# Kernel optimization log

Measured on AMD Instinct MI355X. Metric: run time of the kernel, lower is better.

Reference implementation:

```python
import jax, jax.numpy as jnp
import numpy as np

M, N, D = 8192, 8192, 64

def setup_inputs() -> dict:
    key = jax.random.key(0)
    k1, k2 = jax.random.split(key)
    X = jax.random.normal(k1, (M, D), dtype=jnp.float32)
    Y = jax.random.normal(k2, (N, D), dtype=jnp.float32)
    gamma_param = jnp.asarray(1.0, dtype=jnp.float32)  # learnable scalar (rbf branch)
    return {"X": X, "Y": Y, "gamma_param": gamma_param}

def reference(X, Y, gamma_param):
    # RBF kernel: exp(-gamma * ||x_i - y_j||^2), (m, n)
    x_sq = jnp.sum(X * X, axis=-1)          # (m,)
    y_sq = jnp.sum(Y * Y, axis=-1)          # (n,)
    xy = jnp.einsum("md,nd->mn", X, Y)      # (m, n)
    sq_norm = x_sq[:, None] + y_sq[None, :] - 2.0 * xy
    sq_norm = jnp.maximum(sq_norm, 0.0)     # numerical clamp
    return jnp.exp(-gamma_param * sq_norm)
```

## Files before the change

### kernel.cpp

```cpp
#include <hip/hip_runtime.h>

#define MTOT 8192
#define NTOT 8192
#define DD   64
#define SPLIT (MTOT * DD)

typedef __bf16 bf16x8 __attribute__((ext_vector_type(8)));
typedef float  f32x16 __attribute__((ext_vector_type(16)));
typedef unsigned short u16;
typedef unsigned short u16x4 __attribute__((ext_vector_type(4)));
typedef unsigned short u16x8 __attribute__((ext_vector_type(8)));

__device__ __forceinline__ u16 bf16_rne(float v) {
    unsigned int u = __float_as_uint(v);
    u = u + 0x7FFFu + ((u >> 16) & 1u);
    return (u16)(u >> 16);
}
__device__ __forceinline__ float bf16_to_f32(u16 h) {
    return __uint_as_float(((unsigned int)h) << 16);
}

#define MFMA(a, b, c) __builtin_amdgcn_mfma_f32_32x32x16_bf16((a), (b), (c), 0, 0, 0)

__global__ __launch_bounds__(256)
void rbf_pre_kernel(const float* __restrict__ X, const float* __restrict__ Y,
                    u16* __restrict__ XhiF, u16* __restrict__ XloF,
                    u16* __restrict__ YhiF, u16* __restrict__ YloF,
                    float* __restrict__ xqs, float* __restrict__ yqs)
{
    const int gid = blockIdx.x * 256 + threadIdx.x;
    const int mat = gid >> 15;
    const int r4  = gid & 32767;
    const int row = r4 >> 2;
    const int q   = r4 & 3;
    const float* src = mat ? Y : X;
    u16* hi  = mat ? YhiF : XhiF;
    u16* lo  = mat ? YloF : XloF;
    float* nrm = mat ? yqs : xqs;

    const long rbase = (long)row * DD + q * 16;
    float s = 0.f;
    u16x8 h0, h1, l0, l1;
    #pragma unroll
    for (int c = 0; c < 4; ++c) {
        const float4 v = *reinterpret_cast<const float4*>(src + rbase + c * 4);
        const float vv[4] = {v.x, v.y, v.z, v.w};
        #pragma unroll
        for (int e = 0; e < 4; ++e) {
            const int idx = c * 4 + e;
            const float x = vv[e];
            s = fmaf(x, x, s);
            const u16 hh = bf16_rne(x);
            const u16 ll = bf16_rne(x - bf16_to_f32(hh));
            if (idx < 8) { h0[idx] = hh; l0[idx] = ll; }
            else         { h1[idx - 8] = hh; l1[idx - 8] = ll; }
        }
    }
    s += __shfl_xor(s, 1);
    s += __shfl_xor(s, 2);
    if (q == 0) nrm[row] = s;

    const int tt = row >> 5, lr = row & 31;
    const long fbase = (long)(tt * 4 + q) * 512;
    *reinterpret_cast<u16x8*>(hi + fbase + lr * 8)        = h0;
    *reinterpret_cast<u16x8*>(hi + fbase + (32 + lr) * 8) = h1;
    *reinterpret_cast<u16x8*>(lo + fbase + lr * 8)        = l0;
    *reinterpret_cast<u16x8*>(lo + fbase + (32 + lr) * 8) = l1;
}

__global__ __launch_bounds__(256, 2)
void rbf_rowslab_kernel(const u16* __restrict__ XhiF, const u16* __restrict__ XloF,
                        const u16* __restrict__ YhiF, const u16* __restrict__ YloF,
                        const float* __restrict__ xqs, const float* __restrict__ yqs,
                        const float* __restrict__ gamma_p,
                        float* __restrict__ out)
{
    __shared__ __align__(16) u16 S[4][8192];

    const int t = threadIdx.x;
    const int w = t >> 6;
    const int l = t & 63;
    const int loff = l * 8;

    const int bid = blockIdx.x;
    const int swz = ((bid & 7) << 9) | (bid >> 3);
    const int bm = swz >> 6;
    const int bn = swz & 63;
    const long row0 = (long)bm * 128;
    const long col0 = (long)bn * 128;

    {
        const u16* gsrc;
        if      (w == 0) gsrc = XhiF + (long)bm * 8192;
        else if (w == 1) gsrc = XloF + (long)bm * 8192;
        else if (w == 2) gsrc = YhiF + (long)bn * 8192;
        else             gsrc = YloF + (long)bn * 8192;
        u16* const ldst = &S[w][0];
        #pragma unroll
        for (int c = 0; c < 16; ++c) {
            const int off = c * 512 + loff;
            *reinterpret_cast<int4*>(ldst + off) = *reinterpret_cast<const int4*>(gsrc + off);
        }
    }

    const float g  = gamma_p[0];
    const float g2 = 2.0f * g;
    const int l5x4 = (l >> 5) * 4;
    const int  ln  = l & 31;

    float xv[16];
    #pragma unroll
    for (int q4 = 0; q4 < 4; ++q4) {
        const float4 x4 = *reinterpret_cast<const float4*>(
            xqs + row0 + w * 32 + 8 * q4 + l5x4);
        xv[q4 * 4 + 0] = x4.x; xv[q4 * 4 + 1] = x4.y;
        xv[q4 * 4 + 2] = x4.z; xv[q4 * 4 + 3] = x4.w;
    }
    const float cy0 = -g * yqs[col0 +  0 + ln];
    const float cy1 = -g * yqs[col0 + 32 + ln];
    const float cy2 = -g * yqs[col0 + 64 + ln];
    const float cy3 = -g * yqs[col0 + 96 + ln];

    __syncthreads();

    bf16x8 aH[4], aL[4];
    #pragma unroll
    for (int ks = 0; ks < 4; ++ks) {
        aH[ks] = *reinterpret_cast<const bf16x8*>(&S[0][(w * 4 + ks) * 512 + loff]);
        aL[ks] = *reinterpret_cast<const bf16x8*>(&S[1][(w * 4 + ks) * 512 + loff]);
    }

    f32x16 q0, q1, q2, q3;
    #pragma unroll
    for (int r = 0; r < 16; ++r) { q0[r] = 0.f; q1[r] = 0.f; q2[r] = 0.f; q3[r] = 0.f; }

#define QUAD(ACC, JJ)                                                                   \
    {                                                                                   \
        bf16x8 bh[4], bl[4];                                                            \
        _Pragma("unroll")                                                               \
        for (int ks = 0; ks < 4; ++ks) {                                                \
            bh[ks] = *reinterpret_cast<const bf16x8*>(&S[2][((JJ) * 4 + ks) * 512 + loff]); \
            bl[ks] = *reinterpret_cast<const bf16x8*>(&S[3][((JJ) * 4 + ks) * 512 + loff]); \
        }                                                                               \
        _Pragma("unroll")                                                               \
        for (int ks = 0; ks < 4; ++ks) {                                                \
            ACC = MFMA(aH[ks], bh[ks], ACC);                                            \
            ACC = MFMA(aH[ks], bl[ks], ACC);                                            \
            ACC = MFMA(aL[ks], bh[ks], ACC);                                            \
        }                                                                               \
    }

    QUAD(q0, 0)
    QUAD(q1, 1)
    QUAD(q2, 2)
    QUAD(q3, 3)
#undef QUAD

    float* const obase = out + (row0 + w * 32) * (long)NTOT + col0 + ln;
    #pragma unroll
    for (int r = 0; r < 16; ++r) {
        const int rr = (r & 3) + 8 * (r >> 2) + l5x4;
        float* const orow = obase + rr * (long)NTOT;
        const float nx = -g * xv[r];
        const float a0 = fminf(fmaf(g2, q0[r], nx + cy0), 0.f);
        const float a1 = fminf(fmaf(g2, q1[r], nx + cy1), 0.f);
        const float a2 = fminf(fmaf(g2, q2[r], nx + cy2), 0.f);
        const float a3 = fminf(fmaf(g2, q3[r], nx + cy3), 0.f);
        __builtin_nontemporal_store(__expf(a0), orow);
        __builtin_nontemporal_store(__expf(a1), orow + 32);
        __builtin_nontemporal_store(__expf(a2), orow + 64);
        __builtin_nontemporal_store(__expf(a3), orow + 96);
    }
}

__global__ __launch_bounds__(256, 2)
void rbf_fallback_kernel(const float* __restrict__ X,
                         const float* __restrict__ Y,
                         const float* __restrict__ gamma_p,
                         float* __restrict__ out)
{
    __shared__ unsigned short XfH[4][4][64][8];
    __shared__ unsigned short XfL[4][4][64][8];
    __shared__ unsigned short YfH[4][4][64][8];
    __shared__ unsigned short YfL[4][4][64][8];
    __shared__ float xq[128];
    __shared__ float yq[128];

    const int t = threadIdx.x;
    const long row0 = (long)blockIdx.y * 128;
    const long col0 = (long)blockIdx.x * 128;

    {
        const int k0   = (t & 15) * 4;
        const int ks   = k0 >> 4;
        const int l32  = ((k0 >> 3) & 1) << 5;
        const int slot = k0 & 4;
        #pragma unroll
        for (int i = 0; i < 8; ++i) {
            const int row  = (t >> 4) + i * 16;
            const int mt   = row >> 5;
            const int lane = (row & 31) | l32;
            const float4 vx = *reinterpret_cast<const float4*>(X + (row0 + row) * DD + k0);
            const float4 vy = *reinterpret_cast<const float4*>(Y + (col0 + row) * DD + k0);
            float xv[4] = {vx.x, vx.y, vx.z, vx.w};
            float yv[4] = {vy.x, vy.y, vy.z, vy.w};
            u16x4 xh, xl, yh, yl;
            #pragma unroll
            for (int e = 0; e < 4; ++e) {
                const u16 hx = bf16_rne(xv[e]);
                xh[e] = hx; xl[e] = bf16_rne(xv[e] - bf16_to_f32(hx));
                const u16 hy = bf16_rne(yv[e]);
                yh[e] = hy; yl[e] = bf16_rne(yv[e] - bf16_to_f32(hy));
            }
            *reinterpret_cast<u16x4*>(&XfH[mt][ks][lane][slot]) = xh;
            *reinterpret_cast<u16x4*>(&XfL[mt][ks][lane][slot]) = xl;
            *reinterpret_cast<u16x4*>(&YfH[mt][ks][lane][slot]) = yh;
            *reinterpret_cast<u16x4*>(&YfL[mt][ks][lane][slot]) = yl;
        }
    }
    {
        const int r = t & 127;
        const float* p2 = (t < 128) ? (X + (row0 + r) * DD) : (Y + (col0 + r) * DD);
        float s0 = 0.f, s1 = 0.f, s2 = 0.f, s3 = 0.f;
        #pragma unroll
        for (int c = 0; c < 16; ++c) {
            const float4 v = reinterpret_cast<const float4*>(p2)[c];
            s0 = fmaf(v.x, v.x, s0); s1 = fmaf(v.y, v.y, s1);
            s2 = fmaf(v.z, v.z, s2); s3 = fmaf(v.w, v.w, s3);
        }
        const float s = (s0 + s1) + (s2 + s3);
        if (t < 128) xq[r] = s; else yq[r] = s;
    }
    __syncthreads();

    const int w = t >> 6;
    const int l = t & 63;
    const int mt0 = (w >> 1) * 2;
    const int nt0 = (w & 1) * 2;

    bf16x8 aH[2][4], aL[2][4];
    #pragma unroll
    for (int i = 0; i < 2; ++i)
        #pragma unroll
        for (int ks = 0; ks < 4; ++ks) {
            aH[i][ks] = *reinterpret_cast<const bf16x8*>(&XfH[mt0 + i][ks][l][0]);
            aL[i][ks] = *reinterpret_cast<const bf16x8*>(&XfL[mt0 + i][ks][l][0]);
        }

    f32x16 acc[2][2];
    #pragma unroll
    for (int i = 0; i < 2; ++i)
        #pragma unroll
        for (int j = 0; j < 2; ++j)
            #pragma unroll
            for (int r = 0; r < 16; ++r) acc[i][j][r] = 0.f;

    #pragma unroll
    for (int ks = 0; ks < 4; ++ks) {
        const bf16x8 b0h = *reinterpret_cast<const bf16x8*>(&YfH[nt0 + 0][ks][l][0]);
        const bf16x8 b1h = *reinterpret_cast<const bf16x8*>(&YfH[nt0 + 1][ks][l][0]);
        const bf16x8 b0l = *reinterpret_cast<const bf16x8*>(&YfL[nt0 + 0][ks][l][0]);
        const bf16x8 b1l = *reinterpret_cast<const bf16x8*>(&YfL[nt0 + 1][ks][l][0]);
        acc[0][0] = MFMA(aH[0][ks], b0h, acc[0][0]);
        acc[0][1] = MFMA(aH[0][ks], b1h, acc[0][1]);
        acc[1][0] = MFMA(aH[1][ks], b0h, acc[1][0]);
        acc[1][1] = MFMA(aH[1][ks], b1h, acc[1][1]);
        acc[0][0] = MFMA(aH[0][ks], b0l, acc[0][0]);
        acc[0][1] = MFMA(aH[0][ks], b1l, acc[0][1]);
        acc[1][0] = MFMA(aH[1][ks], b0l, acc[1][0]);
        acc[1][1] = MFMA(aH[1][ks], b1l, acc[1][1]);
        acc[0][0] = MFMA(aL[0][ks], b0h, acc[0][0]);
        acc[0][1] = MFMA(aL[0][ks], b1h, acc[0][1]);
        acc[1][0] = MFMA(aL[1][ks], b0h, acc[1][0]);
        acc[1][1] = MFMA(aL[1][ks], b1h, acc[1][1]);
    }

    const float g = gamma_p[0];
    const int l5x4 = (l >> 5) * 4;
    const int ln = l & 31;
    #pragma unroll
    for (int i = 0; i < 2; ++i) {
        const int mt = mt0 + i;
        float xv[16];
        #pragma unroll
        for (int r = 0; r < 16; ++r)
            xv[r] = xq[mt * 32 + (r & 3) + 8 * (r >> 2) + l5x4];
        #pragma unroll
        for (int j = 0; j < 2; ++j) {
            const int nt = nt0 + j;
            const float yv = yq[nt * 32 + ln];
            const long gr = row0 + mt * 32;
            const long gc = col0 + nt * 32 + ln;
            #pragma unroll
            for (int r = 0; r < 16; ++r) {
                float s = fmaf(-2.f, acc[i][j][r], xv[r] + yv);
                s = fmaxf(s, 0.f);
                const long rr = gr + (r & 3) + 8 * (r >> 2) + l5x4;
                out[rr * NTOT + gc] = __expf(-g * s);
            }
        }
    }
}

extern "C" void kernel_launch(void* const* d_in, const int* in_sizes, int n_in,
                              void* d_out, int out_size, void* d_ws, size_t ws_size,
                              hipStream_t stream) {
    (void)in_sizes; (void)n_in; (void)out_size;
    const float* X = (const float*)d_in[0];
    const float* Y = (const float*)d_in[1];
    const float* gamma_p = (const float*)d_in[2];
    float* out = (float*)d_out;

    const size_t need = 4 * (size_t)SPLIT * sizeof(u16) + (MTOT + NTOT) * sizeof(float);

    if (ws_size >= need) {
        u16* XhiF = (u16*)d_ws;
        u16* XloF = XhiF + SPLIT;
        u16* YhiF = XloF + SPLIT;
        u16* YloF = YhiF + SPLIT;
        float* xqs = (float*)(YloF + SPLIT);
        float* yqs = xqs + MTOT;
        rbf_pre_kernel<<<256, 256, 0, stream>>>(X, Y, XhiF, XloF, YhiF, YloF, xqs, yqs);
        rbf_rowslab_kernel<<<4096, 256, 0, stream>>>(XhiF, XloF, YhiF, YloF, xqs, yqs, gamma_p, out);
    } else {
        dim3 grid(NTOT / 128, MTOT / 128);
        rbf_fallback_kernel<<<grid, 256, 0, stream>>>(X, Y, gamma_p, out);
    }
}
```

Before: 61.74 us.

## Shrink block tile to 64x128 with direct-global A fragments for higher occupancy

Replaces the 128x128 row-slab kernel with a 64x128 tile kernel that stages only the Y hi/lo fragments in shared memory. Each wave loads its X hi/lo fragments directly from global memory and computes a 32x64 sub-tile with two accumulators instead of four. Shared memory per block is halved and the launch bound is raised to 4 blocks per CU, and the grid doubles to 8192 blocks. The aim is more concurrent waves to hide the latency of the output stores, in exchange for more total reads of Y across blocks and less data reuse per block.

```diff
diff --git a/kernel.cpp b/kernel.cpp
--- a/kernel.cpp
+++ b/kernel.cpp
@@ -68,14 +68,14 @@
     *reinterpret_cast<u16x8*>(lo + fbase + (32 + lr) * 8) = l1;
 }
 
-__global__ __launch_bounds__(256, 2)
-void rbf_rowslab_kernel(const u16* __restrict__ XhiF, const u16* __restrict__ XloF,
-                        const u16* __restrict__ YhiF, const u16* __restrict__ YloF,
-                        const float* __restrict__ xqs, const float* __restrict__ yqs,
-                        const float* __restrict__ gamma_p,
-                        float* __restrict__ out)
+__global__ __launch_bounds__(256, 4)
+void rbf_hiocc_kernel(const u16* __restrict__ XhiF, const u16* __restrict__ XloF,
+                      const u16* __restrict__ YhiF, const u16* __restrict__ YloF,
+                      const float* __restrict__ xqs, const float* __restrict__ yqs,
+                      const float* __restrict__ gamma_p,
+                      float* __restrict__ out)
 {
-    __shared__ __align__(16) u16 S[4][8192];
+    __shared__ __align__(16) u16 S[2][8192];
 
     const int t = threadIdx.x;
     const int w = t >> 6;
@@ -83,24 +83,33 @@
     const int loff = l * 8;
 
     const int bid = blockIdx.x;
-    const int swz = ((bid & 7) << 9) | (bid >> 3);
+    const int swz = ((bid & 7) << 10) | (bid >> 3);
     const int bm = swz >> 6;
     const int bn = swz & 63;
-    const long row0 = (long)bm * 128;
+    const long row0 = (long)bm * 64;
     const long col0 = (long)bn * 128;
 
     {
-        const u16* gsrc;
-        if      (w == 0) gsrc = XhiF + (long)bm * 8192;
-        else if (w == 1) gsrc = XloF + (long)bm * 8192;
-        else if (w == 2) gsrc = YhiF + (long)bn * 8192;
-        else             gsrc = YloF + (long)bn * 8192;
-        u16* const ldst = &S[w][0];
-        #pragma unroll
-        for (int c = 0; c < 16; ++c) {
-            const int off = c * 512 + loff;
-            *reinterpret_cast<int4*>(ldst + off) = *reinterpret_cast<const int4*>(gsrc + off);
-        }
+        const u16* const yh = YhiF + (long)bn * 8192;
+        const u16* const yl = YloF + (long)bn * 8192;
+        #pragma unroll
+        for (int cc = 0; cc < 8; ++cc) {
+            const int c = w * 8 + cc;
+            const u16* gsrc = (c < 16) ? (yh + c * 512) : (yl + (c - 16) * 512);
+            u16* ldst = (c < 16) ? &S[0][c * 512] : &S[1][(c - 16) * 512];
+            *reinterpret_cast<int4*>(ldst + loff) = *reinterpret_cast<const int4*>(gsrc + loff);
+        }
+    }
+
+    const int mt  = w & 1;
+    const int nt0 = (w >> 1) * 2;
+
+    const long att = (long)(bm * 2 + mt);
+    bf16x8 aH[4], aL[4];
+    #pragma unroll
+    for (int ks = 0; ks < 4; ++ks) {
+        aH[ks] = *reinterpret_cast<const bf16x8*>(XhiF + (att * 4 + ks) * 512 + loff);
+        aL[ks] = *reinterpret_cast<const bf16x8*>(XloF + (att * 4 + ks) * 512 + loff);
     }
 
     const float g  = gamma_p[0];
@@ -112,64 +121,42 @@
     #pragma unroll
     for (int q4 = 0; q4 < 4; ++q4) {
         const float4 x4 = *reinterpret_cast<const float4*>(
-            xqs + row0 + w * 32 + 8 * q4 + l5x4);
+            xqs + row0 + mt * 32 + 8 * q4 + l5x4);
         xv[q4 * 4 + 0] = x4.x; xv[q4 * 4 + 1] = x4.y;
         xv[q4 * 4 + 2] = x4.z; xv[q4 * 4 + 3] = x4.w;
     }
-    const float cy0 = -g * yqs[col0 +  0 + ln];
-    const float cy1 = -g * yqs[col0 + 32 + ln];
-    const float cy2 = -g * yqs[col0 + 64 + ln];
-    const float cy3 = -g * yqs[col0 + 96 + ln];
+    const float cy0 = -g * yqs[col0 + (nt0 + 0) * 32 + ln];
+    const float cy1 = -g * yqs[col0 + (nt0 + 1) * 32 + ln];
 
     __syncthreads();
 
-    bf16x8 aH[4], aL[4];
+    f32x16 acc0, acc1;
+    #pragma unroll
+    for (int r = 0; r < 16; ++r) { acc0[r] = 0.f; acc1[r] = 0.f; }
+
     #pragma unroll
     for (int ks = 0; ks < 4; ++ks) {
-        aH[ks] = *reinterpret_cast<const bf16x8*>(&S[0][(w * 4 + ks) * 512 + loff]);
-        aL[ks] = *reinterpret_cast<const bf16x8*>(&S[1][(w * 4 + ks) * 512 + loff]);
-    }
-
-    f32x16 q0, q1, q2, q3;
-    #pragma unroll
-    for (int r = 0; r < 16; ++r) { q0[r] = 0.f; q1[r] = 0.f; q2[r] = 0.f; q3[r] = 0.f; }
-
-#define QUAD(ACC, JJ)                                                                   \
-    {                                                                                   \
-        bf16x8 bh[4], bl[4];                                                            \
-        _Pragma("unroll")                                                               \
-        for (int ks = 0; ks < 4; ++ks) {                                                \
-            bh[ks] = *reinterpret_cast<const bf16x8*>(&S[2][((JJ) * 4 + ks) * 512 + loff]); \
-            bl[ks] = *reinterpret_cast<const bf16x8*>(&S[3][((JJ) * 4 + ks) * 512 + loff]); \
-        }                                                                               \
-        _Pragma("unroll")                                                               \
-        for (int ks = 0; ks < 4; ++ks) {                                                \
-            ACC = MFMA(aH[ks], bh[ks], ACC);                                            \
-            ACC = MFMA(aH[ks], bl[ks], ACC);                                            \
-            ACC = MFMA(aL[ks], bh[ks], ACC);                                            \
-        }                                                                               \
-    }
-
-    QUAD(q0, 0)
-    QUAD(q1, 1)
-    QUAD(q2, 2)
-    QUAD(q3, 3)
-#undef QUAD
-
-    float* const obase = out + (row0 + w * 32) * (long)NTOT + col0 + ln;
+        const bf16x8 b0h = *reinterpret_cast<const bf16x8*>(&S[0][((nt0 + 0) * 4 + ks) * 512 + loff]);
+        const bf16x8 b1h = *reinterpret_cast<const bf16x8*>(&S[0][((nt0 + 1) * 4 + ks) * 512 + loff]);
+        const bf16x8 b0l = *reinterpret_cast<const bf16x8*>(&S[1][((nt0 + 0) * 4 + ks) * 512 + loff]);
+        const bf16x8 b1l = *reinterpret_cast<const bf16x8*>(&S[1][((nt0 + 1) * 4 + ks) * 512 + loff]);
+        acc0 = MFMA(aH[ks], b0h, acc0);
+        acc1 = MFMA(aH[ks], b1h, acc1);
+        acc0 = MFMA(aH[ks], b0l, acc0);
+        acc1 = MFMA(aH[ks], b1l, acc1);
+        acc0 = MFMA(aL[ks], b0h, acc0);
+        acc1 = MFMA(aL[ks], b1h, acc1);
+    }
+
+    float* const obase = out + (row0 + mt * 32) * (long)NTOT + col0 + nt0 * 32 + ln;
     #pragma unroll
     for (int r = 0; r < 16; ++r) {
         const int rr = (r & 3) + 8 * (r >> 2) + l5x4;
         float* const orow = obase + rr * (long)NTOT;
-        const float nx = -g * xv[r];
-        const float a0 = fminf(fmaf(g2, q0[r], nx + cy0), 0.f);
-        const float a1 = fminf(fmaf(g2, q1[r], nx + cy1), 0.f);
-        const float a2 = fminf(fmaf(g2, q2[r], nx + cy2), 0.f);
-        const float a3 = fminf(fmaf(g2, q3[r], nx + cy3), 0.f);
+        const float a0 = fminf(fmaf(g2, acc0[r], fmaf(-g, xv[r], cy0)), 0.f);
+        const float a1 = fminf(fmaf(g2, acc1[r], fmaf(-g, xv[r], cy1)), 0.f);
         __builtin_nontemporal_store(__expf(a0), orow);
         __builtin_nontemporal_store(__expf(a1), orow + 32);
-        __builtin_nontemporal_store(__expf(a2), orow + 64);
-        __builtin_nontemporal_store(__expf(a3), orow + 96);
     }
 }
 
@@ -321,7 +308,7 @@
         float* xqs = (float*)(YloF + SPLIT);
         float* yqs = xqs + MTOT;
         rbf_pre_kernel<<<256, 256, 0, stream>>>(X, Y, XhiF, XloF, YhiF, YloF, xqs, yqs);
-        rbf_rowslab_kernel<<<4096, 256, 0, stream>>>(XhiF, XloF, YhiF, YloF, xqs, yqs, gamma_p, out);
+        rbf_hiocc_kernel<<<8192, 256, 0, stream>>>(XhiF, XloF, YhiF, YloF, xqs, yqs, gamma_p, out);
     } else {
         dim3 grid(NTOT / 128, MTOT / 128);
         rbf_fallback_kernel<<<grid, 256, 0, stream>>>(X, Y, gamma_p, out);
```

After: 56.67 us. 8.2% less time.
